# Kernel optimization log

Measured on AMD Instinct MI355X. Metric: run time of the kernel, lower is better.

## Reference

```python
import jax, jax.numpy as jnp
import numpy as np

B, S, D, H = 2, 2048, 1024, 16
DK = D // H


def setup_inputs() -> dict:
    key = jax.random.key(0)
    ks = jax.random.split(key, 9)
    scale = 1.0 / np.sqrt(D)
    inp = {
        "x": jax.random.normal(ks[0], (B, S, D), dtype=jnp.float32),
        "mask": jnp.triu(jnp.ones((S, S), dtype=jnp.int32), k=1),  # 1 = masked (causal)
        "Wq": jax.random.normal(ks[1], (D, D), dtype=jnp.float32) * scale,
        "bq": jnp.zeros((D,), dtype=jnp.float32),
        "Wk": jax.random.normal(ks[2], (D, D), dtype=jnp.float32) * scale,
        "bk": jnp.zeros((D,), dtype=jnp.float32),
        "Wv": jax.random.normal(ks[3], (D, D), dtype=jnp.float32) * scale,
        "bv": jnp.zeros((D,), dtype=jnp.float32),
        "Wo": jax.random.normal(ks[4], (D, D), dtype=jnp.float32) * scale,
        "bo": jnp.zeros((D,), dtype=jnp.float32),
    }
    return inp


def reference(x, mask, Wq, bq, Wk, bk, Wv, bv, Wo, bo):
    # Linear projections (torch nn.Linear: x @ W.T + b; here W stored as (D, D) in
    # (in, out) layout so x @ W + b is equivalent math).
    q = x @ Wq + bq  # (B, S, D)
    k = x @ Wk + bk
    v = x @ Wv + bv
    # Split heads: (B, S, D) -> (B, H, S, DK)
    def split(t):
        return t.reshape(B, S, H, DK).transpose(0, 2, 1, 3)
    q, k, v = split(q), split(k), split(v)
    # Scaled dot-product attention with full score matrix (faithful to original)
    scores = jnp.einsum("bhsd,bhtd->bhst", q, k) / jnp.sqrt(jnp.float32(DK))
    scores = jnp.where(mask[None, None, :, :] == 1, -jnp.inf, scores)
    attn = jax.nn.softmax(scores, axis=-1)  # (B, H, S, S)
    out = jnp.einsum("bhst,bhtd->bhsd", attn, v)
    # Merge heads and final projection
    out = out.transpose(0, 2, 1, 3).reshape(B, S, D)
    return out @ Wo + bo
```

## Files before the change

kernel.cpp:

```cpp
#include <hip/hip_runtime.h>
#include <hip/hip_bf16.h>
#include <cstdint>
#include <cstddef>

typedef __attribute__((ext_vector_type(8))) short short8;
typedef __attribute__((ext_vector_type(4))) float f32x4;
typedef __attribute__((ext_vector_type(4))) unsigned int u32x4;
typedef unsigned short u16;
typedef unsigned int u32;

#define NB 2
#define NS 2048
#define ND 1024
#define NH 16
#define NDK 64

__device__ __forceinline__ u16 f2bf(float f){
  u32 u = __builtin_bit_cast(u32, f);
  u += 0x7fffu + ((u >> 16) & 1u);
  return (u16)(u >> 16);
}

__device__ __forceinline__ u32 pk2(float lo, float hi){
  return (u32)f2bf(lo) | ((u32)f2bf(hi) << 16);
}

__device__ __forceinline__ u32 cvtpk(float lo, float hi){
  u32 r;
  asm("v_cvt_pk_bf16_f32 %0, %1, %2" : "=v"(r) : "v"(lo), "v"(hi));
  return r;
}

__device__ __forceinline__ short8 mk8(ushort4 lo, ushort4 hi){
  short8 r;
  r[0]=(short)lo.x; r[1]=(short)lo.y; r[2]=(short)lo.z; r[3]=(short)lo.w;
  r[4]=(short)hi.x; r[5]=(short)hi.y; r[6]=(short)hi.z; r[7]=(short)hi.w;
  return r;
}

__device__ __forceinline__ void stage16(const u16* g, u16* l, int lane){
#if defined(__has_builtin) && __has_builtin(__builtin_amdgcn_global_load_lds)
  __builtin_amdgcn_global_load_lds(
      (const __attribute__((address_space(1))) u32*)(const void*)g,
      (__attribute__((address_space(3))) u32*)(void*)l, 16, 0, 0);
#else
  ((uint4*)l)[lane] = *(const uint4*)g;
#endif
}


__global__ __launch_bounds__(256) void prep_kernel(
    const float* __restrict__ Wq, const float* __restrict__ Wk,
    const float* __restrict__ Wv, const float* __restrict__ Wo,
    const float* __restrict__ x,
    u16* __restrict__ Wt, u16* __restrict__ xb)
{
  const int z = blockIdx.z;
  const int tx = threadIdx.x, ty = threadIdx.y;
  if (z == 4){
    const int base = ((blockIdx.y*32 + (int)blockIdx.x)*256 + ty*32 + tx)*16;
    float4 v0 = *(const float4*)(x+base);
    float4 v1 = *(const float4*)(x+base+4);
    float4 v2 = *(const float4*)(x+base+8);
    float4 v3 = *(const float4*)(x+base+12);
    u32x4 w0, w1;
    w0[0]=pk2(v0.x,v0.y); w0[1]=pk2(v0.z,v0.w); w0[2]=pk2(v1.x,v1.y); w0[3]=pk2(v1.z,v1.w);
    w1[0]=pk2(v2.x,v2.y); w1[1]=pk2(v2.z,v2.w); w1[2]=pk2(v3.x,v3.y); w1[3]=pk2(v3.z,v3.w);
    *(u32x4*)(xb+base)   = w0;
    *(u32x4*)(xb+base+8) = w1;
    return;
  }
  const float* W = (z==0)?Wq:(z==1)?Wk:(z==2)?Wv:Wo;
  u16* dst = Wt + (size_t)z*ND*ND;
  __shared__ float t[32][33];
  const int n0 = blockIdx.x*32, k0 = blockIdx.y*32;
#pragma unroll
  for (int i=0;i<4;i++) t[ty+i*8][tx] = W[(size_t)(k0+ty+i*8)*ND + n0+tx];
  __syncthreads();
#pragma unroll
  for (int i=0;i<4;i++) dst[(size_t)(n0+ty+i*8)*ND + k0+tx] = f2bf(t[tx][ty+i*8]);
}

template<int MODE>
__global__ __launch_bounds__(256,3) void gemm_kernel(
    const u16* __restrict__ Abf, const u16* __restrict__ Wtz,
    const float* __restrict__ bias0, const float* __restrict__ bias1, const float* __restrict__ bias2,
    u16* __restrict__ Qout, u16* __restrict__ Kout, u16* __restrict__ Vtout,
    float* __restrict__ Fout)
{
  int bx, by;
  if constexpr (MODE==0){
    const int f  = blockIdx.x;
    const int fp = (f & 7)*96 + (f >> 3);
    by = fp / 24; bx = fp % 24;
  } else { bx = blockIdx.x; by = blockIdx.y; }
  const int tid  = threadIdx.x;
  const int lane = tid & 63;
  const int wv   = tid >> 6;
  const int a = lane & 15, g = lane >> 4;
  const int wm = wv >> 1, wn = wv & 1;
  const int m0 = by * 128, n0 = bx * 128;
  const int z  = (MODE==0) ? (n0 >> 10) : 0;

  __shared__ u16 Al[128*64];
  __shared__ u16 Bl[128*64];

  f32x4 acc[4][4] = {};

  const int grow = lane >> 3;
  const int gcol = (lane & 7) * 8;

#pragma unroll 1
  for (int k0 = 0; k0 < ND; k0 += 64) {
    __syncthreads();
#pragma unroll
    for (int i=0;i<4;++i){
      const int r = 32*wv + 8*i + grow;
      const int cs = gcol ^ ((r&7)<<3);
      stage16(Abf + (size_t)(m0+r)*ND + k0 + cs, &Al[(32*wv+8*i)*64], lane);
      stage16(Wtz + (size_t)(n0+r)*ND + k0 + cs, &Bl[(32*wv+8*i)*64], lane);
    }
    __syncthreads();

#pragma unroll
    for (int kk=0; kk<64; kk+=32){
      short8 af[4], bfr[4];
#pragma unroll
      for (int mi=0;mi<4;++mi){
        const int rr = wm*64 + mi*16 + a;
        const int rsw = (rr&7)<<3;
        const u16* rp = &Al[rr*64];
        af[mi] = mk8(*(const ushort4*)(rp + ((kk+4*g)^rsw)),
                     *(const ushort4*)(rp + ((kk+16+4*g)^rsw)));
      }
#pragma unroll
      for (int ni=0;ni<4;++ni){
        const int rr = wn*64 + ni*16 + a;
        const int rsw = (rr&7)<<3;
        const u16* rp = &Bl[rr*64];
        bfr[ni] = mk8(*(const ushort4*)(rp + ((kk+4*g)^rsw)),
                      *(const ushort4*)(rp + ((kk+16+4*g)^rsw)));
      }
      __builtin_amdgcn_s_setprio(1);
#pragma unroll
      for (int mi=0;mi<4;++mi)
#pragma unroll
        for (int ni=0;ni<4;++ni)
          acc[mi][ni] = __builtin_amdgcn_mfma_f32_16x16x32_bf16(af[mi], bfr[ni], acc[mi][ni], 0,0,0);
      __builtin_amdgcn_s_setprio(0);
    }
  }

#pragma unroll
  for (int mi=0;mi<4;++mi){
#pragma unroll
    for (int ni=0;ni<4;++ni){
      const int n  = n0 + wn*64 + ni*16 + a;
      const int mb = m0 + wm*64 + mi*16 + 4*g;
      if constexpr (MODE==0){
        const int nn = n & 1023;
        const float* bp = (z==0)? bias0 : (z==1)? bias1 : bias2;
        const float bias = bp[nn];
        const int h = nn >> 6, dk = nn & 63;
        const int b = mb >> 11, s = mb & 2047;
        if (z==2){
          const int sb = s & 31;
          const int col = (s & ~31) + 8*((sb&15)>>2) + 4*(sb>>4);
          *(uint2*)&Vtout[(((size_t)b*NH + h)*NDK + dk)*NS + col] =
            make_uint2(pk2(acc[mi][ni][0]+bias, acc[mi][ni][1]+bias),
                       pk2(acc[mi][ni][2]+bias, acc[mi][ni][3]+bias));
        } else {
          u16* dst = (z==0)? Qout : Kout;
          const float sc = (z==0)? 0.1803368801111601f : 1.0f;
          const int d5 = dk & 31;
          const int pdk = (dk & 32) + 8*((d5&15)>>2) + (d5&3) + 4*(d5>>4);
#pragma unroll
          for (int r=0;r<4;++r)
            dst[(((size_t)b*NH + h)*NS + (s+r))*NDK + pdk] = f2bf((acc[mi][ni][r]+bias)*sc);
        }
      } else {
        const float bias = bias0[n];
#pragma unroll
        for (int r=0;r<4;++r)
          Fout[(size_t)(mb+r)*ND + n] = acc[mi][ni][r] + bias;
      }
    }
  }
}

#define KOFF(p_, q_) ((p_)*8192 + (q_)*4096)
#define VOFF(p_, q_) (16384 + (p_)*8192 + (q_)*4096)
#define FIXM 10.0f

__global__ __launch_bounds__(512,4) void attn_kernel(
    const u16* __restrict__ Qg, const u16* __restrict__ Kg,
    const u16* __restrict__ Vtg, u16* __restrict__ Og)
{
  const int tid  = threadIdx.x;
  const int lane = tid & 63, wv = tid >> 6;
  const int qw = wv & 3, par = wv >> 2;
  const int a = lane & 15, g = lane >> 4;
  const int bh = blockIdx.x;
  const int qt = blockIdx.y;
  const int qb = (qt < 8) ? qt : (23 - qt);
  const int qB  = qb * 128;
  const int q0w = qB + qw*32;
  const int nr  = qb + 1;

  __shared__ u16 SH[32768];

  short8 qf[2][2];
#pragma unroll
  for (int qi=0; qi<2; ++qi){
    const u16* qptr = Qg + ((size_t)bh*NS + q0w + qi*16 + a)*NDK;
    qf[qi][0] = *(const short8*)(qptr + 8*g);
    qf[qi][1] = *(const short8*)(qptr + 32 + 8*g);
  }

  float ls[2] = {0.f, 0.f};
  f32x4 accO[4][2] = {};

  const int srow = wv*8 + (lane >> 3);
  const int scol = (lane & 7) * 8;
  const int scs  = scol ^ ((srow & 7) << 3);
  const u16* kgp = Kg  + (size_t)bh*NS*NDK + (size_t)srow*NDK + scs;
  const u16* vgp = Vtg + (size_t)bh*NDK*NS + (size_t)srow*NS  + scs;

  stage16(kgp,            &SH[KOFF(0,0) + wv*512], lane);
  stage16(kgp + 64*NDK,   &SH[KOFF(0,1) + wv*512], lane);
  stage16(vgp,            &SH[VOFF(0,0) + wv*512], lane);
  stage16(vgp + 64,       &SH[VOFF(0,1) + wv*512], lane);
  __syncthreads();

  const u16* kstg = kgp + 128*NDK;
  const u16* vstg = vgp + 128;

  int cur = 0;
#pragma unroll 1
  for (int r=0; r<nr; ++r){
    const int t = 2*r + par;
    const int kv0 = t * 64;
    if (r+1 < nr){
      stage16(kstg,          &SH[KOFF(cur^1,0) + wv*512], lane);
      stage16(kstg + 64*NDK, &SH[KOFF(cur^1,1) + wv*512], lane);
      stage16(vstg,          &SH[VOFF(cur^1,0) + wv*512], lane);
      stage16(vstg + 64,     &SH[VOFF(cur^1,1) + wv*512], lane);
      kstg += 128*NDK; vstg += 128;
    }

    if (kv0 <= q0w + 31){
      const u16* Kb = &SH[KOFF(cur,par)];
      const u16* Vb = &SH[VOFF(cur,par)];
      f32x4 sc[2][4] = {};
      __builtin_amdgcn_s_setprio(1);
#pragma unroll
      for (int kvf=0; kvf<4; ++kvf){
        const int rr = kvf*16 + a;
        const int rsw = (rr&7)<<3;
        const u16* rp = Kb + rr*64;
        short8 kf0 = *(const short8*)(rp + ((8*g) ^ rsw));
        short8 kf1 = *(const short8*)(rp + ((32 + 8*g) ^ rsw));
#pragma unroll
        for (int qi=0; qi<2; ++qi){
          sc[qi][kvf] = __builtin_amdgcn_mfma_f32_16x16x32_bf16(kf0, qf[qi][0], sc[qi][kvf], 0,0,0);
          sc[qi][kvf] = __builtin_amdgcn_mfma_f32_16x16x32_bf16(kf1, qf[qi][1], sc[qi][kvf], 0,0,0);
        }
      }
      __builtin_amdgcn_s_setprio(0);

      const bool dm = (kv0 + 63 > q0w);
      short8 pf[2][2];
#pragma unroll
      for (int qi=0; qi<2; ++qi){
        const int q = q0w + qi*16 + a;
        if (dm){
#pragma unroll
          for (int kvf=0;kvf<4;++kvf)
#pragma unroll
            for (int rr=0;rr<4;++rr){
              const int kv = kv0 + kvf*16 + 4*g + rr;
              if (kv > q) sc[qi][kvf][rr] = -1e30f;
            }
        }
        float rsum = 0.f;
        u32 pw[2][4];
#pragma unroll
        for (int kvf=0;kvf<4;++kvf){
          const float e0 = exp2f(sc[qi][kvf][0] - FIXM);
          const float e1 = exp2f(sc[qi][kvf][1] - FIXM);
          const float e2 = exp2f(sc[qi][kvf][2] - FIXM);
          const float e3 = exp2f(sc[qi][kvf][3] - FIXM);
          rsum += (e0+e1)+(e2+e3);
          pw[kvf>>1][(kvf&1)*2+0] = cvtpk(e0,e1);
          pw[kvf>>1][(kvf&1)*2+1] = cvtpk(e2,e3);
        }
        pf[qi][0] = __builtin_bit_cast(short8, *(u32x4*)pw[0]);
        pf[qi][1] = __builtin_bit_cast(short8, *(u32x4*)pw[1]);
        rsum += __shfl_xor(rsum,16);
        rsum += __shfl_xor(rsum,32);
        ls[qi] += rsum;
      }

      __builtin_amdgcn_s_setprio(1);
#pragma unroll
      for (int dkg=0;dkg<4;++dkg){
        const int rr = dkg*16 + a;
        const int rsw = (rr&7)<<3;
        const u16* rp = Vb + rr*64;
        short8 vf0 = *(const short8*)(rp + ((8*g) ^ rsw));
        short8 vf1 = *(const short8*)(rp + ((32 + 8*g) ^ rsw));
#pragma unroll
        for (int qi=0; qi<2; ++qi){
          accO[dkg][qi] = __builtin_amdgcn_mfma_f32_16x16x32_bf16(vf0, pf[qi][0], accO[dkg][qi], 0,0,0);
          accO[dkg][qi] = __builtin_amdgcn_mfma_f32_16x16x32_bf16(vf1, pf[qi][1], accO[dkg][qi], 0,0,0);
        }
      }
      __builtin_amdgcn_s_setprio(0);
    }

    __syncthreads();
    cur ^= 1;
  }

  float* ms = (float*)SH;
  if (par == 1){
#pragma unroll
    for (int qi=0; qi<2; ++qi){
      const int idx = (((qw*64 + lane)*2) + qi)*17;
#pragma unroll
      for (int dkg=0;dkg<4;++dkg)
#pragma unroll
        for (int j=0;j<4;++j) ms[idx + dkg*4 + j] = accO[dkg][qi][j];
      ms[idx+16] = ls[qi];
    }
  }
  __syncthreads();

  if (par == 0){
    u16* Lw = &SH[18432] + qw*2048;
#pragma unroll
    for (int qi=0; qi<2; ++qi){
      const int idx = (((qw*64 + lane)*2) + qi)*17;
      const float linv = 1.0f / (ls[qi] + ms[idx+16]);
      const int row = qi*16 + a;
#pragma unroll
      for (int dkg=0; dkg<4; ++dkg){
        const int col = dkg*16 + 4*g;
        const float o0 = (accO[dkg][qi][0] + ms[idx+dkg*4+0])*linv;
        const float o1 = (accO[dkg][qi][1] + ms[idx+dkg*4+1])*linv;
        const float o2 = (accO[dkg][qi][2] + ms[idx+dkg*4+2])*linv;
        const float o3 = (accO[dkg][qi][3] + ms[idx+dkg*4+3])*linv;
        *(uint2*)&Lw[(row<<6) + (col ^ ((row&7)<<3))] = make_uint2(cvtpk(o0,o1), cvtpk(o2,o3));
      }
    }
    const int b = bh >> 4, h = bh & 15;
#pragma unroll
    for (int j=0; j<4; ++j){
      const int row = j*8 + (lane>>3);
      const int cc  = (lane&7)*8;
      uint4 d = *(const uint4*)&Lw[(row<<6) + (cc ^ ((row&7)<<3))];
      *(uint4*)(Og + ((size_t)b*NS + qB + qw*32 + row)*ND + h*NDK + cc) = d;
    }
  }
}

extern "C" void kernel_launch(void* const* d_in, const int* in_sizes, int n_in,
                              void* d_out, int out_size, void* d_ws, size_t ws_size,
                              hipStream_t stream) {
  (void)in_sizes; (void)n_in; (void)out_size; (void)ws_size;
  const float* x  = (const float*)d_in[0];
  const float* Wq = (const float*)d_in[2];
  const float* bq = (const float*)d_in[3];
  const float* Wk = (const float*)d_in[4];
  const float* bk = (const float*)d_in[5];
  const float* Wv = (const float*)d_in[6];
  const float* bv = (const float*)d_in[7];
  const float* Wo = (const float*)d_in[8];
  const float* bo = (const float*)d_in[9];
  float* out = (float*)d_out;

  u16* Wt  = (u16*)d_ws;
  u16* Qb  = Wt  + (size_t)4194304;
  u16* Kb  = Qb  + (size_t)4194304;
  u16* Vtb = Kb  + (size_t)4194304;
  u16* XO  = Vtb + (size_t)4194304;

  prep_kernel<<<dim3(32,32,5), dim3(32,8,1), 0, stream>>>(Wq, Wk, Wv, Wo, x, Wt, XO);
  gemm_kernel<0><<<dim3(768), dim3(256), 0, stream>>>(
      XO, Wt, bq, bk, bv, Qb, Kb, Vtb, (float*)nullptr);
  attn_kernel<<<dim3(32,16), dim3(512), 0, stream>>>(Qb, Kb, Vtb, XO);
  gemm_kernel<1><<<dim3(8,32), dim3(256), 0, stream>>>(
      XO, Wt + (size_t)3*1048576, bo, nullptr, nullptr,
      (u16*)nullptr, (u16*)nullptr, (u16*)nullptr, out);
}
```

Before: 111.8 us.

## Permute K-dimension storage so GEMM fragments load as single 16-byte LDS reads

The bf16 copies of x, the transposed weights and the attention output are now written with a permuted column order inside each 32-element K block. With that order, each lane's eight MFMA operand elements sit next to each other, so the GEMM inner loop reads them with one short8 LDS load instead of two ushort4 loads plus repacking. The permutation is applied to both operands' K dimension, so the dot products stay the same. The cost is less contiguous global stores in the prep and epilogue code.

```diff
diff --git a/kernel.cpp b/kernel.cpp
--- a/kernel.cpp
+++ b/kernel.cpp
@@ -28,13 +28,6 @@
 __device__ __forceinline__ u32 cvtpk(float lo, float hi){
   u32 r;
   asm("v_cvt_pk_bf16_f32 %0, %1, %2" : "=v"(r) : "v"(lo), "v"(hi));
-  return r;
-}
-
-__device__ __forceinline__ short8 mk8(ushort4 lo, ushort4 hi){
-  short8 r;
-  r[0]=(short)lo.x; r[1]=(short)lo.y; r[2]=(short)lo.z; r[3]=(short)lo.w;
-  r[4]=(short)hi.x; r[5]=(short)hi.y; r[6]=(short)hi.z; r[7]=(short)hi.w;
   return r;
 }
 
@@ -63,22 +56,24 @@
     float4 v1 = *(const float4*)(x+base+4);
     float4 v2 = *(const float4*)(x+base+8);
     float4 v3 = *(const float4*)(x+base+12);
-    u32x4 w0, w1;
-    w0[0]=pk2(v0.x,v0.y); w0[1]=pk2(v0.z,v0.w); w0[2]=pk2(v1.x,v1.y); w0[3]=pk2(v1.z,v1.w);
-    w1[0]=pk2(v2.x,v2.y); w1[1]=pk2(v2.z,v2.w); w1[2]=pk2(v3.x,v3.y); w1[3]=pk2(v3.z,v3.w);
-    *(u32x4*)(xb+base)   = w0;
-    *(u32x4*)(xb+base+8) = w1;
+    const int blk = base & ~31;
+    const int h4  = (base & 16) ? 4 : 0;
+    *(uint2*)(xb + blk +  0 + h4) = make_uint2(pk2(v0.x,v0.y), pk2(v0.z,v0.w));
+    *(uint2*)(xb + blk +  8 + h4) = make_uint2(pk2(v1.x,v1.y), pk2(v1.z,v1.w));
+    *(uint2*)(xb + blk + 16 + h4) = make_uint2(pk2(v2.x,v2.y), pk2(v2.z,v2.w));
+    *(uint2*)(xb + blk + 24 + h4) = make_uint2(pk2(v3.x,v3.y), pk2(v3.z,v3.w));
     return;
   }
   const float* W = (z==0)?Wq:(z==1)?Wk:(z==2)?Wv:Wo;
   u16* dst = Wt + (size_t)z*ND*ND;
   __shared__ float t[32][33];
   const int n0 = blockIdx.x*32, k0 = blockIdx.y*32;
+  const int ptx = 8*((tx&15)>>2) + (tx&3) + 4*(tx>>4);
 #pragma unroll
   for (int i=0;i<4;i++) t[ty+i*8][tx] = W[(size_t)(k0+ty+i*8)*ND + n0+tx];
   __syncthreads();
 #pragma unroll
-  for (int i=0;i<4;i++) dst[(size_t)(n0+ty+i*8)*ND + k0+tx] = f2bf(t[tx][ty+i*8]);
+  for (int i=0;i<4;i++) dst[(size_t)(n0+ty+i*8)*ND + k0+ptx] = f2bf(t[tx][ty+i*8]);
 }
 
 template<int MODE>
@@ -129,17 +124,13 @@
       for (int mi=0;mi<4;++mi){
         const int rr = wm*64 + mi*16 + a;
         const int rsw = (rr&7)<<3;
-        const u16* rp = &Al[rr*64];
-        af[mi] = mk8(*(const ushort4*)(rp + ((kk+4*g)^rsw)),
-                     *(const ushort4*)(rp + ((kk+16+4*g)^rsw)));
+        af[mi] = *(const short8*)(&Al[rr*64] + ((kk + 8*g) ^ rsw));
       }
 #pragma unroll
       for (int ni=0;ni<4;++ni){
         const int rr = wn*64 + ni*16 + a;
         const int rsw = (rr&7)<<3;
-        const u16* rp = &Bl[rr*64];
-        bfr[ni] = mk8(*(const ushort4*)(rp + ((kk+4*g)^rsw)),
-                      *(const ushort4*)(rp + ((kk+16+4*g)^rsw)));
+        bfr[ni] = *(const short8*)(&Bl[rr*64] + ((kk + 8*g) ^ rsw));
       }
       __builtin_amdgcn_s_setprio(1);
 #pragma unroll
@@ -345,12 +336,12 @@
       const int row = qi*16 + a;
 #pragma unroll
       for (int dkg=0; dkg<4; ++dkg){
-        const int col = dkg*16 + 4*g;
+        const int pcol = 32*(dkg>>1) + 8*g + 4*(dkg&1);
         const float o0 = (accO[dkg][qi][0] + ms[idx+dkg*4+0])*linv;
         const float o1 = (accO[dkg][qi][1] + ms[idx+dkg*4+1])*linv;
         const float o2 = (accO[dkg][qi][2] + ms[idx+dkg*4+2])*linv;
         const float o3 = (accO[dkg][qi][3] + ms[idx+dkg*4+3])*linv;
-        *(uint2*)&Lw[(row<<6) + (col ^ ((row&7)<<3))] = make_uint2(cvtpk(o0,o1), cvtpk(o2,o3));
+        *(uint2*)&Lw[(row<<6) + (pcol ^ ((row&7)<<3))] = make_uint2(cvtpk(o0,o1), cvtpk(o2,o3));
       }
     }
     const int b = bh >> 4, h = bh & 15;
```

Measured after the change: 107.2 us. -4.1%, faster.
